# Kernel tuning notes

Hardware: AMD Instinct MI355X
Metric: run time of the kernel (lower is better)

## Reference

```python
import jax, jax.numpy as jnp
import numpy as np

N_WORDS, N_BOOKS, L_WORD = 256, 8, 64
TAU_SQ = 5.0
B = 32768


def setup_inputs() -> dict:
    key = jax.random.key(0)
    ks = jax.random.split(key, 4)
    f = jax.random.normal(ks[0], (B, N_BOOKS * L_WORD), jnp.float32)
    # codebooks: xavier_uniform over (N_words, N_books*L_word)
    lim_c = float(np.sqrt(6.0 / (N_WORDS + N_BOOKS * L_WORD)))
    codebooks = jax.random.uniform(ks[1], (N_WORDS, N_BOOKS * L_WORD), jnp.float32, -lim_c, lim_c)
    # mlp[0]: Linear(L_word, 4*L_word), weights ~ N(0, 0.01)
    W1 = jax.random.normal(ks[2], (L_WORD, 4 * L_WORD), jnp.float32) * 0.01
    b1 = jnp.zeros((4 * L_WORD,), jnp.float32)
    # mlp[2]: Linear(4*L_word, N_books), xavier_uniform
    lim2 = float(np.sqrt(6.0 / (4 * L_WORD + N_BOOKS)))
    W2 = jax.random.uniform(ks[3], (4 * L_WORD, N_BOOKS), jnp.float32, -lim2, lim2)
    b2 = jnp.zeros((N_BOOKS,), jnp.float32)
    return dict(f=f, codebooks=codebooks, W1=W1, b1=b1, W2=W2, b2=b2)


def reference(f, codebooks, W1, b1, W2, b2):
    Bsz = f.shape[0]
    # --- soft_quantization: per-book squared distances -> softmax -> weighted codewords ---
    x = f.reshape(Bsz, N_BOOKS, L_WORD)               # (B, K, L)
    c = codebooks.reshape(N_WORDS, N_BOOKS, L_WORD)   # (W, K, L)
    # squared euclidean distance per book: (B, K, W)
    d = (jnp.sum(x * x, axis=-1)[:, :, None]
         - 2.0 * jnp.einsum('bkl,wkl->bkw', x, c)
         + jnp.sum(c * c, axis=-1).T[None, :, :])
    p = jax.nn.softmax(-TAU_SQ * d, axis=-1)          # (B, K, W) soft assignments
    z = jnp.einsum('bkw,wkl->bkl', p, c).reshape(Bsz, N_BOOKS * L_WORD)
    p_flat = p.reshape(Bsz, N_BOOKS * N_WORDS)        # concat over books along dim 1
    # --- codebook-index classifier MLP on per-book splits ---
    f_split = f.reshape(-1, L_WORD)                   # (B*K, L)
    h = jax.nn.relu(f_split @ W1 + b1)                # (B*K, 4L)
    logits_codebook = jax.nn.log_softmax(h @ W2 + b2, axis=1)  # (B*K, N_books)
    return f, z, p_flat, logits_codebook
```

## Files before the change

kernel.cpp:

```cpp
#include <hip/hip_runtime.h>

typedef __fp16   pk16x2 __attribute__((ext_vector_type(2)));
typedef _Float16 f16x4 __attribute__((ext_vector_type(4)));
typedef _Float16 f16x8 __attribute__((ext_vector_type(8)));
typedef float    f32x16 __attribute__((ext_vector_type(16)));

static constexpr int BSZ = 32768;
static constexpr int NB  = 8;
static constexpr int NW  = 256;
static constexpr int LW  = 64;
static constexpr int DF  = 512;
#define TAU   5.0f
#define LOG2E 1.44269504088896f
#define LN2   0.69314718055994f

union U2 { pk16x2 h; unsigned u; };
union U8 { f16x8 v; unsigned u[4]; };
union U4 { f16x4 v; unsigned u[2]; };
union F4 { float4 v; float a[4]; };

__device__ inline unsigned pku(float a, float b) {
    U2 c; c.h = __builtin_amdgcn_cvt_pkrtz(a, b); return c.u;
}
__device__ inline pk16x2 pkh(float a, float b) {
    return __builtin_amdgcn_cvt_pkrtz(a, b);
}

__global__ __launch_bounds__(256, 2) void quant_kernel(
    const float* __restrict__ f, const float* __restrict__ cb,
    float* __restrict__ out_z, float* __restrict__ out_p)
{
    __shared__ _Float16 ct [NW * LW];
    __shared__ _Float16 ctt[LW * NW];
    __shared__ float    ccs[NW];

    const int k    = blockIdx.y;
    const int r0   = blockIdx.x * 128;
    const int tid  = threadIdx.x;
    const int wid  = tid >> 6;
    const int lane = tid & 63;
    const int lr   = lane & 31;
    const int hi   = lane >> 5;
    const int row  = r0 + wid * 32 + lr;

    float x_[32];
    {
        const float* fr = f + (size_t)row * DF + k * LW + hi * 8;
        #pragma unroll
        for (int i = 0; i < 8; ++i)
            *(float4*)&x_[i * 4] = *(const float4*)(fr + (i >> 1) * 16 + (i & 1) * 4);
    }

    {
        const float* cw = cb + (size_t)tid * DF + k * LW;
        float c_[64];
        #pragma unroll
        for (int i = 0; i < 16; ++i)
            *(float4*)&c_[i * 4] = *(const float4*)(cw + i * 4);
        float cc = 0.f;
        #pragma unroll
        for (int l = 0; l < 64; ++l) cc += c_[l] * c_[l];
        ccs[tid] = cc;
        #pragma unroll
        for (int c8 = 0; c8 < 8; ++c8) {
            U8 u;
            #pragma unroll
            for (int m = 0; m < 4; ++m)
                u.u[m] = pku(c_[c8 * 8 + 2 * m], c_[c8 * 8 + 2 * m + 1]);
            *(f16x8*)&ct[tid * 64 + (c8 ^ (tid & 7)) * 8] = u.v;
            #pragma unroll
            for (int j = 0; j < 8; ++j) {
                int l = c8 * 8 + j;
                ctt[l * 256 + (((tid >> 3) ^ (l & 7))) * 8 + (tid & 7)] = (_Float16)c_[l];
            }
        }
    }

    f16x8 bxh[4], bxl[4];
    #pragma unroll
    for (int ks = 0; ks < 4; ++ks) {
        U8 uh, ul;
        #pragma unroll
        for (int m = 0; m < 4; ++m) {
            float a = x_[ks * 8 + 2 * m], b = x_[ks * 8 + 2 * m + 1];
            pk16x2 ph = pkh(a, b);
            U2 c; c.h = ph;
            uh.u[m] = c.u;
            ul.u[m] = pku(a - (float)ph[0], b - (float)ph[1]);
        }
        bxh[ks] = uh.v; bxl[ks] = ul.v;
    }

    __syncthreads();

    f32x16 acc[8];
    #pragma unroll
    for (int wt = 0; wt < 8; ++wt) acc[wt] = {};
    #pragma unroll
    for (int wt = 0; wt < 8; ++wt) {
        const int w = wt * 32 + lr;
        #pragma unroll
        for (int ks = 0; ks < 4; ++ks) {
            f16x8 a = *(const f16x8*)&ct[w * 64 + (((ks * 2 + hi) ^ (lr & 7))) * 8];
            acc[wt] = __builtin_amdgcn_mfma_f32_32x32x16_f16(a, bxh[ks], acc[wt], 0, 0, 0);
            acc[wt] = __builtin_amdgcn_mfma_f32_32x32x16_f16(a, bxl[ks], acc[wt], 0, 0, 0);
        }
    }

    const float KK = TAU * LOG2E;
    float mx = -1e30f;
    #pragma unroll
    for (int wt = 0; wt < 8; ++wt) {
        #pragma unroll
        for (int g = 0; g < 4; ++g) {
            F4 cc4; cc4.v = *(const float4*)&ccs[wt * 32 + g * 8 + hi * 4];
            #pragma unroll
            for (int j = 0; j < 4; ++j) {
                int q = g * 4 + j;
                float li = (2.f * acc[wt][q] - cc4.a[j]) * KK;
                acc[wt][q] = li;
                mx = fmaxf(mx, li);
            }
        }
    }
    mx = fmaxf(mx, __shfl_xor(mx, 32));
    float s = 0.f;
    #pragma unroll
    for (int wt = 0; wt < 8; ++wt) {
        #pragma unroll
        for (int q = 0; q < 16; ++q) {
            float e = __builtin_amdgcn_exp2f(acc[wt][q] - mx);
            acc[wt][q] = e; s += e;
        }
    }
    s += __shfl_xor(s, 32);
    const float inv = 1.f / s;
    #pragma unroll
    for (int wt = 0; wt < 8; ++wt) {
        #pragma unroll
        for (int q = 0; q < 16; ++q) acc[wt][q] *= inv;
    }

    float* prow = out_p + (size_t)row * (NB * NW) + (size_t)k * NW + hi * 8;
    f32x16 zacc[2];
    zacc[0] = {}; zacc[1] = {};
    #pragma unroll
    for (int ks = 0; ks < 16; ++ks) {
        const int wt = ks >> 1;
        const int q0 = (ks & 1) * 8;
        float v[8];
        #pragma unroll
        for (int i = 0; i < 4; ++i) {
            float a0 = acc[wt][q0 + i];
            float a1 = acc[wt][q0 + 4 + i];
            float snd = hi ? a0 : a1;
            float rcv = __shfl_xor(snd, 32);
            v[i]     = hi ? rcv : a0;
            v[4 + i] = hi ? a1 : rcv;
        }
        *(float4*)(prow + ks * 16)     = float4{v[0], v[1], v[2], v[3]};
        *(float4*)(prow + ks * 16 + 4) = float4{v[4], v[5], v[6], v[7]};
        U8 pa;
        pa.u[0] = pku(v[0], v[1]); pa.u[1] = pku(v[2], v[3]);
        pa.u[2] = pku(v[4], v[5]); pa.u[3] = pku(v[6], v[7]);
        #pragma unroll
        for (int nt = 0; nt < 2; ++nt) {
            const int l = nt * 32 + lr;
            f16x8 bz = *(const f16x8*)&ctt[l * 256 + (((ks * 2 + hi) ^ (lr & 7))) * 8];
            zacc[nt] = __builtin_amdgcn_mfma_f32_32x32x16_f16(pa.v, bz, zacc[nt], 0, 0, 0);
        }
    }

    #pragma unroll
    for (int nt = 0; nt < 2; ++nt) {
        #pragma unroll
        for (int q = 0; q < 16; ++q) {
            int rr = (q & 3) + 8 * (q >> 2) + 4 * hi;
            out_z[(size_t)(r0 + wid * 32 + rr) * DF + k * LW + nt * 32 + lr] = zacc[nt][q];
        }
    }
}

__global__ __launch_bounds__(256, 2) void mlp_kernel(
    const float* __restrict__ f, const float* __restrict__ W1,
    const float* __restrict__ b1, const float* __restrict__ W2,
    const float* __restrict__ b2, float* __restrict__ out_f,
    float* __restrict__ out_lg)
{
    __shared__ _Float16 w1t[NW * LW];
    __shared__ _Float16 xs [128 * LW];
    __shared__ _Float16 w2t[8 * NW];
    __shared__ float    b1s[NW];
    __shared__ float    b2s[8];

    const int tid  = threadIdx.x;
    const int wid  = tid >> 6;
    const int lane = tid & 63;
    const int lr   = lane & 31;
    const int hi   = lane >> 5;
    const size_t m0 = (size_t)blockIdx.x * 128;

    #pragma unroll
    for (int i = 0; i < 8; ++i) {
        int c = i * 256 + tid;
        int r = c >> 4, l4 = c & 15;
        float4 v = *(const float4*)(f + m0 * LW + (size_t)c * 4);
        *(float4*)(out_f + m0 * LW + (size_t)c * 4) = v;
        U4 w; w.u[0] = pku(v.x, v.y); w.u[1] = pku(v.z, v.w);
        *(f16x4*)&xs[r * 64 + (((l4 >> 1) ^ (r & 7))) * 8 + (l4 & 1) * 4] = w.v;
    }
    {
        float wv[64];
        #pragma unroll
        for (int l = 0; l < 64; ++l) wv[l] = W1[l * 256 + tid];
        #pragma unroll
        for (int c8 = 0; c8 < 8; ++c8) {
            U8 u;
            #pragma unroll
            for (int m = 0; m < 4; ++m)
                u.u[m] = pku(wv[c8 * 8 + 2 * m], wv[c8 * 8 + 2 * m + 1]);
            *(f16x8*)&w1t[tid * 64 + (c8 ^ (tid & 7)) * 8] = u.v;
        }
    }
    {
        int m = tid >> 5, c = tid & 31;
        U8 u;
        #pragma unroll
        for (int mm = 0; mm < 4; ++mm)
            u.u[mm] = pku(W2[(c * 8 + 2 * mm) * 8 + m], W2[(c * 8 + 2 * mm + 1) * 8 + m]);
        *(f16x8*)&w2t[m * 256 + (c ^ m) * 8] = u.v;
    }
    b1s[tid] = b1[tid];
    if (tid < 8) b2s[tid] = b2[tid];
    __syncthreads();

    f16x8 bx[4];
    #pragma unroll
    for (int ks = 0; ks < 4; ++ks)
        bx[ks] = *(const f16x8*)&xs[(wid * 32 + lr) * 64 + (((ks * 2 + hi) ^ (lr & 7))) * 8];

    f32x16 acc1[8];
    #pragma unroll
    for (int ht = 0; ht < 8; ++ht) acc1[ht] = {};
    #pragma unroll
    for (int ht = 0; ht < 8; ++ht) {
        const int h = ht * 32 + lr;
        #pragma unroll
        for (int ks = 0; ks < 4; ++ks) {
            f16x8 a = *(const f16x8*)&w1t[h * 64 + (((ks * 2 + hi) ^ (lr & 7))) * 8];
            acc1[ht] = __builtin_amdgcn_mfma_f32_32x32x16_f16(a, bx[ks], acc1[ht], 0, 0, 0);
        }
    }
    #pragma unroll
    for (int ht = 0; ht < 8; ++ht) {
        #pragma unroll
        for (int g = 0; g < 4; ++g) {
            F4 b4; b4.v = *(const float4*)&b1s[ht * 32 + g * 8 + hi * 4];
            #pragma unroll
            for (int j = 0; j < 4; ++j) {
                int q = g * 4 + j;
                acc1[ht][q] = fmaxf(acc1[ht][q] + b4.a[j], 0.f);
            }
        }
    }

    f32x16 acc2 = {};
    #pragma unroll
    for (int ks = 0; ks < 16; ++ks) {
        const int ht = ks >> 1;
        const int q0 = (ks & 1) * 8;
        float v[8];
        #pragma unroll
        for (int i = 0; i < 4; ++i) {
            float a0 = acc1[ht][q0 + i];
            float a1 = acc1[ht][q0 + 4 + i];
            float snd = hi ? a0 : a1;
            float rcv = __shfl_xor(snd, 32);
            v[i]     = hi ? rcv : a0;
            v[4 + i] = hi ? a1 : rcv;
        }
        U8 hb;
        hb.u[0] = pku(v[0], v[1]); hb.u[1] = pku(v[2], v[3]);
        hb.u[2] = pku(v[4], v[5]); hb.u[3] = pku(v[6], v[7]);
        f16x8 aw2 = *(const f16x8*)&w2t[(lr & 7) * 256 + (((ks * 2 + hi) ^ (lr & 7))) * 8];
        acc2 = __builtin_amdgcn_mfma_f32_32x32x16_f16(aw2, hb.v, acc2, 0, 0, 0);
    }

    F4 b2v; b2v.v = *(const float4*)&b2s[hi * 4];
    float lg[4];
    #pragma unroll
    for (int q = 0; q < 4; ++q) lg[q] = acc2[q] + b2v.a[q];
    float m = fmaxf(fmaxf(lg[0], lg[1]), fmaxf(lg[2], lg[3]));
    m = fmaxf(m, __shfl_xor(m, 32));
    float se = 0.f;
    #pragma unroll
    for (int q = 0; q < 4; ++q) se += __builtin_amdgcn_exp2f((lg[q] - m) * LOG2E);
    se += __shfl_xor(se, 32);
    float lse = m + __builtin_amdgcn_logf(se) * LN2;
    float4 o = float4{lg[0] - lse, lg[1] - lse, lg[2] - lse, lg[3] - lse};
    *(float4*)(out_lg + (m0 + wid * 32 + lr) * 8 + hi * 4) = o;
}

extern "C" void kernel_launch(void* const* d_in, const int* in_sizes, int n_in,
                              void* d_out, int out_size, void* d_ws, size_t ws_size,
                              hipStream_t stream) {
    const float* f  = (const float*)d_in[0];
    const float* cb = (const float*)d_in[1];
    const float* W1 = (const float*)d_in[2];
    const float* b1 = (const float*)d_in[3];
    const float* W2 = (const float*)d_in[4];
    const float* b2 = (const float*)d_in[5];

    float* out    = (float*)d_out;
    float* out_f  = out;
    float* out_z  = out_f + (size_t)BSZ * DF;
    float* out_p  = out_z + (size_t)BSZ * DF;
    float* out_lg = out_p + (size_t)BSZ * NB * NW;

    hipLaunchKernelGGL(quant_kernel, dim3(BSZ / 128, NB), dim3(256), 0, stream,
                       f, cb, out_z, out_p);
    hipLaunchKernelGGL(mlp_kernel, dim3(BSZ * NB / 128), dim3(256), 0, stream,
                       f, W1, b1, W2, b2, out_f, out_lg);
}
```

Measured before the change: 188.6 us.

## Fuse quantization and MLP kernels with precomputed fp16 weights in workspace

Adds a small prep kernel that converts the codebooks, their transpose, squared norms, W1 and W2 to fp16 in workspace once per call. The quantization and MLP work are merged into one kernel that reads f only once, reuses the fp16 split of x for the MLP GEMM, and writes out_f from the same load. Per-block LDS staging and the __syncthreads are dropped, so MFMA operands now come straight from global/L2 instead of shared memory. This removes the second pass over f and the repeated per-block weight conversion, but raises register pressure in the fused kernel and relies on cache for operand reuse.

```diff
diff --git a/kernel.cpp b/kernel.cpp
--- a/kernel.cpp
+++ b/kernel.cpp
@@ -1,7 +1,6 @@
 #include <hip/hip_runtime.h>
 
 typedef __fp16   pk16x2 __attribute__((ext_vector_type(2)));
-typedef _Float16 f16x4 __attribute__((ext_vector_type(4)));
 typedef _Float16 f16x8 __attribute__((ext_vector_type(8)));
 typedef float    f32x16 __attribute__((ext_vector_type(16)));
 
@@ -16,63 +15,98 @@
 
 union U2 { pk16x2 h; unsigned u; };
 union U8 { f16x8 v; unsigned u[4]; };
-union U4 { f16x4 v; unsigned u[2]; };
 union F4 { float4 v; float a[4]; };
 
 __device__ inline unsigned pku(float a, float b) {
     U2 c; c.h = __builtin_amdgcn_cvt_pkrtz(a, b); return c.u;
 }
-__device__ inline pk16x2 pkh(float a, float b) {
-    return __builtin_amdgcn_cvt_pkrtz(a, b);
-}
-
-__global__ __launch_bounds__(256, 2) void quant_kernel(
-    const float* __restrict__ f, const float* __restrict__ cb,
-    float* __restrict__ out_z, float* __restrict__ out_p)
+
+static constexpr size_t WS_CBH = 0;
+static constexpr size_t WS_CBT = 262144;
+static constexpr size_t WS_CC  = 524288;
+static constexpr size_t WS_W1H = 532480;
+static constexpr size_t WS_W2H = 565248;
+
+__global__ __launch_bounds__(256) void prep_kernel(
+    const float* __restrict__ cb, const float* __restrict__ W1,
+    const float* __restrict__ W2, char* __restrict__ ws)
 {
-    __shared__ _Float16 ct [NW * LW];
-    __shared__ _Float16 ctt[LW * NW];
-    __shared__ float    ccs[NW];
+    _Float16* cbh = (_Float16*)(ws + WS_CBH);
+    _Float16* cbt = (_Float16*)(ws + WS_CBT);
+    float*    cc  = (float*)   (ws + WS_CC);
+    _Float16* w1h = (_Float16*)(ws + WS_W1H);
+    _Float16* w2h = (_Float16*)(ws + WS_W2H);
+    const int b = blockIdx.x, t = threadIdx.x;
+
+    if (b < 8) {
+        const float* src = cb + (size_t)t * DF + b * LW;
+        float c_[64];
+        #pragma unroll
+        for (int i = 0; i < 16; ++i)
+            *(float4*)&c_[i * 4] = *(const float4*)(src + i * 4);
+        float s = 0.f;
+        #pragma unroll
+        for (int l = 0; l < 64; ++l) s += c_[l] * c_[l];
+        cc[b * 256 + t] = s;
+        #pragma unroll
+        for (int c8 = 0; c8 < 8; ++c8) {
+            U8 u;
+            #pragma unroll
+            for (int m = 0; m < 4; ++m)
+                u.u[m] = pku(c_[c8 * 8 + 2 * m], c_[c8 * 8 + 2 * m + 1]);
+            *(f16x8*)&cbh[((size_t)(b * 256 + t)) * 64 + c8 * 8] = u.v;
+        }
+        #pragma unroll
+        for (int l = 0; l < 64; ++l)
+            cbt[((size_t)(b * 64 + l)) * 256 + t] = (_Float16)c_[l];
+    } else {
+        float wv[64];
+        #pragma unroll
+        for (int l = 0; l < 64; ++l) wv[l] = W1[l * 256 + t];
+        #pragma unroll
+        for (int c8 = 0; c8 < 8; ++c8) {
+            U8 u;
+            #pragma unroll
+            for (int m = 0; m < 4; ++m)
+                u.u[m] = pku(wv[c8 * 8 + 2 * m], wv[c8 * 8 + 2 * m + 1]);
+            *(f16x8*)&w1h[(size_t)t * 64 + c8 * 8] = u.v;
+        }
+        const int c = t >> 5, h0 = (t & 31) * 8;
+        #pragma unroll
+        for (int j = 0; j < 8; ++j)
+            w2h[c * 256 + h0 + j] = (_Float16)W2[(h0 + j) * 8 + c];
+    }
+}
+
+__global__ __launch_bounds__(256, 2) void fused_kernel(
+    const float* __restrict__ f, const char* __restrict__ ws,
+    const float* __restrict__ b1, const float* __restrict__ b2,
+    float* __restrict__ out_f, float* __restrict__ out_z,
+    float* __restrict__ out_p, float* __restrict__ out_lg)
+{
+    const _Float16* cbh = (const _Float16*)(ws + WS_CBH);
+    const _Float16* cbt = (const _Float16*)(ws + WS_CBT);
+    const float*    cc  = (const float*)   (ws + WS_CC);
+    const _Float16* w1h = (const _Float16*)(ws + WS_W1H);
+    const _Float16* w2h = (const _Float16*)(ws + WS_W2H);
 
     const int k    = blockIdx.y;
-    const int r0   = blockIdx.x * 128;
     const int tid  = threadIdx.x;
     const int wid  = tid >> 6;
     const int lane = tid & 63;
     const int lr   = lane & 31;
     const int hi   = lane >> 5;
-    const int row  = r0 + wid * 32 + lr;
+    const int row  = blockIdx.x * 128 + wid * 32 + lr;
 
     float x_[32];
     {
-        const float* fr = f + (size_t)row * DF + k * LW + hi * 8;
-        #pragma unroll
-        for (int i = 0; i < 8; ++i)
-            *(float4*)&x_[i * 4] = *(const float4*)(fr + (i >> 1) * 16 + (i & 1) * 4);
-    }
-
-    {
-        const float* cw = cb + (size_t)tid * DF + k * LW;
-        float c_[64];
-        #pragma unroll
-        for (int i = 0; i < 16; ++i)
-            *(float4*)&c_[i * 4] = *(const float4*)(cw + i * 4);
-        float cc = 0.f;
-        #pragma unroll
-        for (int l = 0; l < 64; ++l) cc += c_[l] * c_[l];
-        ccs[tid] = cc;
-        #pragma unroll
-        for (int c8 = 0; c8 < 8; ++c8) {
-            U8 u;
-            #pragma unroll
-            for (int m = 0; m < 4; ++m)
-                u.u[m] = pku(c_[c8 * 8 + 2 * m], c_[c8 * 8 + 2 * m + 1]);
-            *(f16x8*)&ct[tid * 64 + (c8 ^ (tid & 7)) * 8] = u.v;
-            #pragma unroll
-            for (int j = 0; j < 8; ++j) {
-                int l = c8 * 8 + j;
-                ctt[l * 256 + (((tid >> 3) ^ (l & 7))) * 8 + (tid & 7)] = (_Float16)c_[l];
-            }
+        const float* fr = f     + (size_t)row * DF + k * LW + hi * 8;
+        float*       fo = out_f + (size_t)row * DF + k * LW + hi * 8;
+        #pragma unroll
+        for (int i = 0; i < 8; ++i) {
+            float4 v = *(const float4*)(fr + (i >> 1) * 16 + (i & 1) * 4);
+            *(float4*)&x_[i * 4] = v;
+            *(float4*)(fo + (i >> 1) * 16 + (i & 1) * 4) = v;
         }
     }
 
@@ -83,7 +117,7 @@
         #pragma unroll
         for (int m = 0; m < 4; ++m) {
             float a = x_[ks * 8 + 2 * m], b = x_[ks * 8 + 2 * m + 1];
-            pk16x2 ph = pkh(a, b);
+            pk16x2 ph = __builtin_amdgcn_cvt_pkrtz(a, b);
             U2 c; c.h = ph;
             uh.u[m] = c.u;
             ul.u[m] = pku(a - (float)ph[0], b - (float)ph[1]);
@@ -91,29 +125,28 @@
         bxh[ks] = uh.v; bxl[ks] = ul.v;
     }
 
-    __syncthreads();
-
+    const _Float16* ca = cbh + (size_t)k * NW * LW;
     f32x16 acc[8];
     #pragma unroll
     for (int wt = 0; wt < 8; ++wt) acc[wt] = {};
     #pragma unroll
     for (int wt = 0; wt < 8; ++wt) {
-        const int w = wt * 32 + lr;
         #pragma unroll
         for (int ks = 0; ks < 4; ++ks) {
-            f16x8 a = *(const f16x8*)&ct[w * 64 + (((ks * 2 + hi) ^ (lr & 7))) * 8];
+            f16x8 a = *(const f16x8*)(ca + (size_t)(wt * 32 + lr) * 64 + ks * 16 + hi * 8);
             acc[wt] = __builtin_amdgcn_mfma_f32_32x32x16_f16(a, bxh[ks], acc[wt], 0, 0, 0);
             acc[wt] = __builtin_amdgcn_mfma_f32_32x32x16_f16(a, bxl[ks], acc[wt], 0, 0, 0);
         }
     }
 
+    const float* ccb = cc + k * NW;
     const float KK = TAU * LOG2E;
     float mx = -1e30f;
     #pragma unroll
     for (int wt = 0; wt < 8; ++wt) {
         #pragma unroll
         for (int g = 0; g < 4; ++g) {
-            F4 cc4; cc4.v = *(const float4*)&ccs[wt * 32 + g * 8 + hi * 4];
+            F4 cc4; cc4.v = *(const float4*)&ccb[wt * 32 + g * 8 + hi * 4];
             #pragma unroll
             for (int j = 0; j < 4; ++j) {
                 int q = g * 4 + j;
@@ -142,6 +175,7 @@
     }
 
     float* prow = out_p + (size_t)row * (NB * NW) + (size_t)k * NW + hi * 8;
+    const _Float16* cz = cbt + (size_t)k * LW * NW;
     f32x16 zacc[2];
     zacc[0] = {}; zacc[1] = {};
     #pragma unroll
@@ -165,97 +199,36 @@
         pa.u[2] = pku(v[4], v[5]); pa.u[3] = pku(v[6], v[7]);
         #pragma unroll
         for (int nt = 0; nt < 2; ++nt) {
-            const int l = nt * 32 + lr;
-            f16x8 bz = *(const f16x8*)&ctt[l * 256 + (((ks * 2 + hi) ^ (lr & 7))) * 8];
+            f16x8 bz = *(const f16x8*)(cz + (size_t)(nt * 32 + lr) * 256 + ks * 16 + hi * 8);
             zacc[nt] = __builtin_amdgcn_mfma_f32_32x32x16_f16(pa.v, bz, zacc[nt], 0, 0, 0);
         }
     }
-
+    const int rbase = blockIdx.x * 128 + wid * 32;
     #pragma unroll
     for (int nt = 0; nt < 2; ++nt) {
         #pragma unroll
         for (int q = 0; q < 16; ++q) {
             int rr = (q & 3) + 8 * (q >> 2) + 4 * hi;
-            out_z[(size_t)(r0 + wid * 32 + rr) * DF + k * LW + nt * 32 + lr] = zacc[nt][q];
-        }
-    }
-}
-
-__global__ __launch_bounds__(256, 2) void mlp_kernel(
-    const float* __restrict__ f, const float* __restrict__ W1,
-    const float* __restrict__ b1, const float* __restrict__ W2,
-    const float* __restrict__ b2, float* __restrict__ out_f,
-    float* __restrict__ out_lg)
-{
-    __shared__ _Float16 w1t[NW * LW];
-    __shared__ _Float16 xs [128 * LW];
-    __shared__ _Float16 w2t[8 * NW];
-    __shared__ float    b1s[NW];
-    __shared__ float    b2s[8];
-
-    const int tid  = threadIdx.x;
-    const int wid  = tid >> 6;
-    const int lane = tid & 63;
-    const int lr   = lane & 31;
-    const int hi   = lane >> 5;
-    const size_t m0 = (size_t)blockIdx.x * 128;
-
-    #pragma unroll
-    for (int i = 0; i < 8; ++i) {
-        int c = i * 256 + tid;
-        int r = c >> 4, l4 = c & 15;
-        float4 v = *(const float4*)(f + m0 * LW + (size_t)c * 4);
-        *(float4*)(out_f + m0 * LW + (size_t)c * 4) = v;
-        U4 w; w.u[0] = pku(v.x, v.y); w.u[1] = pku(v.z, v.w);
-        *(f16x4*)&xs[r * 64 + (((l4 >> 1) ^ (r & 7))) * 8 + (l4 & 1) * 4] = w.v;
-    }
-    {
-        float wv[64];
-        #pragma unroll
-        for (int l = 0; l < 64; ++l) wv[l] = W1[l * 256 + tid];
-        #pragma unroll
-        for (int c8 = 0; c8 < 8; ++c8) {
-            U8 u;
-            #pragma unroll
-            for (int m = 0; m < 4; ++m)
-                u.u[m] = pku(wv[c8 * 8 + 2 * m], wv[c8 * 8 + 2 * m + 1]);
-            *(f16x8*)&w1t[tid * 64 + (c8 ^ (tid & 7)) * 8] = u.v;
-        }
-    }
-    {
-        int m = tid >> 5, c = tid & 31;
-        U8 u;
-        #pragma unroll
-        for (int mm = 0; mm < 4; ++mm)
-            u.u[mm] = pku(W2[(c * 8 + 2 * mm) * 8 + m], W2[(c * 8 + 2 * mm + 1) * 8 + m]);
-        *(f16x8*)&w2t[m * 256 + (c ^ m) * 8] = u.v;
-    }
-    b1s[tid] = b1[tid];
-    if (tid < 8) b2s[tid] = b2[tid];
-    __syncthreads();
-
-    f16x8 bx[4];
-    #pragma unroll
-    for (int ks = 0; ks < 4; ++ks)
-        bx[ks] = *(const f16x8*)&xs[(wid * 32 + lr) * 64 + (((ks * 2 + hi) ^ (lr & 7))) * 8];
+            out_z[(size_t)(rbase + rr) * DF + k * LW + nt * 32 + lr] = zacc[nt][q];
+        }
+    }
 
     f32x16 acc1[8];
     #pragma unroll
     for (int ht = 0; ht < 8; ++ht) acc1[ht] = {};
     #pragma unroll
     for (int ht = 0; ht < 8; ++ht) {
-        const int h = ht * 32 + lr;
         #pragma unroll
         for (int ks = 0; ks < 4; ++ks) {
-            f16x8 a = *(const f16x8*)&w1t[h * 64 + (((ks * 2 + hi) ^ (lr & 7))) * 8];
-            acc1[ht] = __builtin_amdgcn_mfma_f32_32x32x16_f16(a, bx[ks], acc1[ht], 0, 0, 0);
+            f16x8 a = *(const f16x8*)(w1h + (size_t)(ht * 32 + lr) * 64 + ks * 16 + hi * 8);
+            acc1[ht] = __builtin_amdgcn_mfma_f32_32x32x16_f16(a, bxh[ks], acc1[ht], 0, 0, 0);
         }
     }
     #pragma unroll
     for (int ht = 0; ht < 8; ++ht) {
         #pragma unroll
         for (int g = 0; g < 4; ++g) {
-            F4 b4; b4.v = *(const float4*)&b1s[ht * 32 + g * 8 + hi * 4];
+            F4 b4; b4.v = *(const float4*)&b1[ht * 32 + g * 8 + hi * 4];
             #pragma unroll
             for (int j = 0; j < 4; ++j) {
                 int q = g * 4 + j;
@@ -282,11 +255,11 @@
         U8 hb;
         hb.u[0] = pku(v[0], v[1]); hb.u[1] = pku(v[2], v[3]);
         hb.u[2] = pku(v[4], v[5]); hb.u[3] = pku(v[6], v[7]);
-        f16x8 aw2 = *(const f16x8*)&w2t[(lr & 7) * 256 + (((ks * 2 + hi) ^ (lr & 7))) * 8];
+        f16x8 aw2 = *(const f16x8*)(w2h + (size_t)(lr & 7) * 256 + ks * 16 + hi * 8);
         acc2 = __builtin_amdgcn_mfma_f32_32x32x16_f16(aw2, hb.v, acc2, 0, 0, 0);
     }
 
-    F4 b2v; b2v.v = *(const float4*)&b2s[hi * 4];
+    F4 b2v; b2v.v = *(const float4*)&b2[hi * 4];
     float lg[4];
     #pragma unroll
     for (int q = 0; q < 4; ++q) lg[q] = acc2[q] + b2v.a[q];
@@ -297,8 +270,8 @@
     for (int q = 0; q < 4; ++q) se += __builtin_amdgcn_exp2f((lg[q] - m) * LOG2E);
     se += __shfl_xor(se, 32);
     float lse = m + __builtin_amdgcn_logf(se) * LN2;
-    float4 o = float4{lg[0] - lse, lg[1] - lse, lg[2] - lse, lg[3] - lse};
-    *(float4*)(out_lg + (m0 + wid * 32 + lr) * 8 + hi * 4) = o;
+    *(float4*)(out_lg + (size_t)row * 64 + k * 8 + hi * 4) =
+        float4{lg[0] - lse, lg[1] - lse, lg[2] - lse, lg[3] - lse};
 }
 
 extern "C" void kernel_launch(void* const* d_in, const int* in_sizes, int n_in,
@@ -317,8 +290,8 @@
     float* out_p  = out_z + (size_t)BSZ * DF;
     float* out_lg = out_p + (size_t)BSZ * NB * NW;
 
-    hipLaunchKernelGGL(quant_kernel, dim3(BSZ / 128, NB), dim3(256), 0, stream,
-                       f, cb, out_z, out_p);
-    hipLaunchKernelGGL(mlp_kernel, dim3(BSZ * NB / 128), dim3(256), 0, stream,
-                       f, W1, b1, W2, b2, out_f, out_lg);
-}
+    hipLaunchKernelGGL(prep_kernel, dim3(9), dim3(256), 0, stream,
+                       cb, W1, W2, (char*)d_ws);
+    hipLaunchKernelGGL(fused_kernel, dim3(BSZ / 128, NB), dim3(256), 0, stream,
+                       f, (const char*)d_ws, b1, b2, out_f, out_z, out_p, out_lg);
+}
```

Result: slower. 258.8 us (+37.2%).
